# Optimization experiments

Hardware: AMD Instinct MI355X
Metric: run time of the kernel (lower is better)

## Reference

```python
import jax, jax.numpy as jnp
import numpy as np

N, S, E, H = 8, 1024, 1024, 16
DK = E // H

def setup_inputs() -> dict:
    key = jax.random.key(0)
    ks = jax.random.split(key, 10)
    s = 1.0 / np.sqrt(E)
    x = jax.random.normal(ks[0], (N, S, E), dtype=jnp.float32)
    attn_mask = jax.random.randint(ks[1], (N, S, S), 0, 2) == 1
    Wq = jax.random.normal(ks[2], (E, E), dtype=jnp.float32) * s
    Wk = jax.random.normal(ks[3], (E, E), dtype=jnp.float32) * s
    Wv = jax.random.normal(ks[4], (E, E), dtype=jnp.float32) * s
    Wo = jax.random.normal(ks[5], (E, E), dtype=jnp.float32) * s
    bq = jax.random.normal(ks[6], (E,), dtype=jnp.float32) * s
    bk = jax.random.normal(ks[7], (E,), dtype=jnp.float32) * s
    bv = jax.random.normal(ks[8], (E,), dtype=jnp.float32) * s
    bo = jax.random.normal(ks[9], (E,), dtype=jnp.float32) * s
    return {"x": x, "attn_mask": attn_mask, "Wq": Wq, "bq": bq, "Wk": Wk, "bk": bk,
            "Wv": Wv, "bv": bv, "Wo": Wo, "bo": bo}

def reference(x, attn_mask, Wq, bq, Wk, bk, Wv, bv, Wo, bo):
    n, s, e = x.shape
    # projections, split into heads: (N, H, S, DK)
    q = (x @ Wq + bq).reshape(n, s, H, DK).transpose(0, 2, 1, 3)
    k = (x @ Wk + bk).reshape(n, s, H, DK).transpose(0, 2, 1, 3)
    v = (x @ Wv + bv).reshape(n, s, H, DK).transpose(0, 2, 1, 3)
    logits = jnp.einsum("nhqd,nhkd->nhqk", q, k) / np.sqrt(DK).astype(np.float32)
    # mask==True positions are suppressed (masked_fill with -1e9)
    logits = jnp.where(attn_mask[:, None, :, :], jnp.float32(-1e9), logits)
    attn = jax.nn.softmax(logits, axis=-1)  # exp(log_softmax) == softmax
    o = jnp.einsum("nhqk,nhkd->nhqd", attn, v)
    o = o.transpose(0, 2, 1, 3).reshape(n, s, e)
    return o @ Wo + bo
```

## Files before the change

kernel.cpp:

```cpp
#include <hip/hip_runtime.h>
#include <hip/hip_bf16.h>

typedef unsigned short u16;
typedef unsigned int   u32;
typedef unsigned long long u64;

#define SEQ 1024
#define EMB 1024
#define NH  16
#define DKH 64

#define QSCALE 0.18033688f
#define SCLAMP 43.3f

typedef __attribute__((ext_vector_type(8))) short short8;
typedef __attribute__((ext_vector_type(4))) float floatx4;

__device__ __forceinline__ float b2f(u16 u) {
  return __uint_as_float(((u32)u) << 16);
}
__device__ __forceinline__ u16 f2b(float f) {
  u32 u = __float_as_uint(f);
  u32 r = u + 0x7fffu + ((u >> 16) & 1u);
  return (u16)(r >> 16);
}

__device__ __forceinline__ void glds16(const u16* g, u16* l) {
  __builtin_amdgcn_global_load_lds(
      (const __attribute__((address_space(1))) u32*)g,
      (__attribute__((address_space(3))) u32*)l, 16, 0, 0);
}

__global__ __launch_bounds__(256) void probe_inputs(const u32* __restrict__ A,
                                                    const u32* __restrict__ B,
                                                    int* __restrict__ flags) {
  __shared__ int mA, mB, mBig, xB16;
  if (threadIdx.x == 0) { mA = 0; mB = 0; mBig = 0; xB16 = 0; }
  __syncthreads();
  int la = 0, lb = 0;
  for (int i = threadIdx.x; i < 4096; i += 256) {
    if ((A[i] & 0xFEFEFEFEu) == 0) la++;
    if ((B[i] & 0xFEFEFEFEu) == 0) lb++;
  }
  atomicAdd(&mA, la); atomicAdd(&mB, lb);
  __syncthreads();
  const int xIsB = (mA > mB) ? 1 : 0;
  const u32* X = xIsB ? B : A;
  const u32* M = xIsB ? A : B;
  int big = 0, cnt = 0;
  for (int i = threadIdx.x; i < 4096; i += 256)
    if (M[i] > 1u) big = 1;
  for (int i = threadIdx.x; i < 2048; i += 256) {
    u16 v = (u16)(X[i] & 0xffffu);
    int e = (v >> 7) & 0xFF;
    if (e >= 110 && e <= 135) cnt++;
  }
  if (big) atomicOr(&mBig, 1);
  atomicAdd(&xB16, cnt);
  __syncthreads();
  if (threadIdx.x == 0) {
    flags[0] = xIsB;
    flags[1] = (xB16 > 1500) ? 1 : 0;
    flags[2] = mBig;
  }
}

__global__ __launch_bounds__(256) void convert_x(const void* __restrict__ bigA,
                                                 const void* __restrict__ bigB,
                                                 const int* __restrict__ flags,
                                                 u16* __restrict__ out) {
  const void* x = flags[0] ? bigB : bigA;
  int i = (blockIdx.x * 256 + threadIdx.x) * 4;
  if (flags[1]) {
    *(ushort4*)(out + i) = *(const ushort4*)((const u16*)x + i);
  } else {
    float4 v = *(const float4*)((const float*)x + i);
    ushort4 o;
    o.x = f2b(v.x); o.y = f2b(v.y); o.z = f2b(v.z); o.w = f2b(v.w);
    *(ushort4*)(out + i) = o;
  }
}

__global__ __launch_bounds__(256) void build_maskbits(const void* __restrict__ bigA,
                                                      const void* __restrict__ bigB,
                                                      const int* __restrict__ flags,
                                                      u32* __restrict__ out) {
  const void* mask = flags[0] ? bigA : bigB;
  const int mbyte = flags[2];
  const int t = threadIdx.x;
  const int lane = t & 63, w = t >> 6;
  const u64 base0 = (u64)blockIdx.x * 8192;
#pragma unroll 4
  for (int k = 0; k < 32; k++) {
    u64 idx = base0 + k * 256 + t;
    int v;
    if (mbyte) v = ((const unsigned char*)mask)[idx] == 0;
    else       v = ((const u32*)mask)[idx] == 0;
    u64 b = __ballot(v);
    if (lane == 0) {
      u64 wbase = (base0 + k * 256 + w * 64) >> 5;
      out[wbase]     = (u32)b;
      out[wbase + 1] = (u32)(b >> 32);
    }
  }
}

__global__ __launch_bounds__(256) void transpose_convert_w4(
    const void* __restrict__ w0, const void* __restrict__ w1,
    const void* __restrict__ w2, const void* __restrict__ w3,
    u16* __restrict__ outQKV, u16* __restrict__ outO,
    const int* __restrict__ flags) {
  __shared__ float tile[32][33];
  const int z = blockIdx.z;
  const void* in = (z == 0) ? w0 : (z == 1) ? w1 : (z == 2) ? w2 : w3;
  u16* out = (z < 3) ? (outQKV + (u64)z * EMB * EMB) : outO;
  const float scale = (z == 0) ? QSCALE : 1.0f;
  const int amode = flags[1];
  const int tx = threadIdx.x & 31;
  const int ty = threadIdx.x >> 5;
  const int bx = blockIdx.x * 32, by = blockIdx.y * 32;
  if (amode) {
    const u16* inb = (const u16*)in;
#pragma unroll
    for (int r = ty; r < 32; r += 8)
      tile[r][tx] = b2f(inb[(u64)(by + r) * EMB + bx + tx]);
  } else {
    const float* inf = (const float*)in;
#pragma unroll
    for (int r = ty; r < 32; r += 8)
      tile[r][tx] = inf[(u64)(by + r) * EMB + bx + tx];
  }
  __syncthreads();
#pragma unroll
  for (int r = ty; r < 32; r += 8)
    out[(u64)(bx + r) * EMB + by + tx] = f2b(tile[tx][r] * scale);
}

__global__ __launch_bounds__(256) void convert_biases(const void* b0, const void* b1,
                                                      const void* b2, const void* b3,
                                                      float* __restrict__ out,
                                                      const int* __restrict__ flags) {
  const void* ptrs[4] = {b0, b1, b2, b3};
  const void* p = ptrs[blockIdx.x];
  const float scale = (blockIdx.x == 0) ? QSCALE : 1.0f;
  const int amode = flags[1];
  for (int i = threadIdx.x; i < 1024; i += 256) {
    float v = amode ? b2f(((const u16*)p)[i]) : ((const float*)p)[i];
    out[blockIdx.x * 1024 + i] = v * scale;
  }
}

#define VTP 65
__global__ __launch_bounds__(256) void transpose_v(const u16* __restrict__ in,
                                                   u16* __restrict__ out) {
  __shared__ u16 tile[64 * VTP];
  const int t = threadIdx.x;
  const int s0 = blockIdx.x * 64;
  const u64 off = (u64)blockIdx.y * SEQ * DKH;
  const int row = t >> 2, c0 = (t & 3) * 16;
  const u16* ip = in + off + (u64)(s0 + row) * DKH + c0;
  *(uint4*)(&tile[row * VTP + c0])     = *(const uint4*)(ip);
  *(uint4*)(&tile[row * VTP + c0 + 8]) = *(const uint4*)(ip + 8);
  __syncthreads();
  const int d = t >> 2;
  u16 buf[16];
#pragma unroll
  for (int j = 0; j < 16; j++) buf[j] = tile[(c0 + j) * VTP + d];
  u16* op = out + off + (u64)d * SEQ + s0 + c0;
  *(uint4*)(op)     = *(uint4*)(&buf[0]);
  *(uint4*)(op + 8) = *(uint4*)(&buf[8]);
}


template <int OUTMODE>
__device__ __forceinline__ void gemm_core(
    const u16* __restrict__ X, const u16* __restrict__ Wt,
    const float* __restrict__ bias,
    u16* __restrict__ Qg, u16* __restrict__ Kg, u16* __restrict__ Vh,
    float* __restrict__ outf, int row0) {
  __shared__ __align__(16) u16 lds[2][(256 + 128) * 64];
  const int t = threadIdx.x;
  const int lane = t & 63;
  const int w = t >> 6;
  const int wr = w >> 1, wc = w & 1;
  const int l15 = lane & 15, l4 = lane >> 4;
  const int bM = blockIdx.x * 256, bN = blockIdx.y * 128;
  const int r7 = l15 & 7;
  const int cA = (l4 ^ r7) << 3;
  const int cB = (l4 ^ r7 ^ 4) << 3;

  floatx4 acc[4][4];
#pragma unroll
  for (int i = 0; i < 4; i++)
#pragma unroll
    for (int j = 0; j < 4; j++)
      acc[i][j] = (floatx4){0.f, 0.f, 0.f, 0.f};

  const int srow = w * 8 + (lane >> 3);
  const int schk = ((lane & 7) ^ (lane >> 3)) << 3;
  const u16* Ap = X + (u64)(row0 + bM + srow) * EMB + schk;
  const u16* Bp = Wt + (u64)(bN + srow) * EMB + schk;
  u16* Ad0 = &lds[0][w * 512];
  u16* Bd0 = &lds[0][16384 + w * 512];
  u16* Ad1 = &lds[1][w * 512];
  u16* Bd1 = &lds[1][16384 + w * 512];

  auto stage = [&](u16* Ad, u16* Bd, int k0) {
    glds16(Ap + k0, Ad);
    glds16(Ap + k0 + 64 * EMB, Ad + 4096);
    glds16(Ap + k0 + 128 * EMB, Ad + 8192);
    glds16(Ap + k0 + 192 * EMB, Ad + 12288);
    glds16(Bp + k0, Bd);
    glds16(Bp + k0 + 64 * EMB, Bd + 4096);
  };

  auto compute = [&](const u16* __restrict__ Ab, const u16* __restrict__ Bb) {
    short8 bf[4][2];
#pragma unroll
    for (int n = 0; n < 4; n++) {
      const int gr = (wc * 64 + n * 16 + l15) * 64;
      bf[n][0] = *(const short8*)(&Bb[gr + cA]);
      bf[n][1] = *(const short8*)(&Bb[gr + cB]);
    }
#pragma unroll
    for (int mh = 0; mh < 2; mh++) {
      short8 af[2][2];
#pragma unroll
      for (int m = 0; m < 2; m++) {
        const int fr = (wr * 64 + mh * 32 + m * 16 + l15) * 64;
        af[m][0] = *(const short8*)(&Ab[fr + cA]);
        af[m][1] = *(const short8*)(&Ab[fr + cB]);
      }
      __builtin_amdgcn_s_setprio(1);
#pragma unroll
      for (int m = 0; m < 2; m++)
#pragma unroll
        for (int n = 0; n < 4; n++) {
          acc[mh * 2 + m][n] = __builtin_amdgcn_mfma_f32_16x16x32_bf16(
              af[m][0], bf[n][0], acc[mh * 2 + m][n], 0, 0, 0);
          acc[mh * 2 + m][n] = __builtin_amdgcn_mfma_f32_16x16x32_bf16(
              af[m][1], bf[n][1], acc[mh * 2 + m][n], 0, 0, 0);
        }
      __builtin_amdgcn_s_setprio(0);
    }
  };

  stage(Ad0, Bd0, 0);
  for (int k0 = 0; k0 < EMB; k0 += 128) {
    stage(Ad1, Bd1, k0 + 64);
    asm volatile("s_waitcnt vmcnt(6)" ::: "memory");
    asm volatile("s_barrier" ::: "memory");
    compute(&lds[0][0], &lds[0][16384]);
    asm volatile("s_barrier" ::: "memory");
    if (k0 + 128 < EMB) {
      stage(Ad0, Bd0, k0 + 128);
      asm volatile("s_waitcnt vmcnt(6)" ::: "memory");
    } else {
      asm volatile("s_waitcnt vmcnt(0)" ::: "memory");
    }
    asm volatile("s_barrier" ::: "memory");
    compute(&lds[1][0], &lds[1][16384]);
    asm volatile("s_barrier" ::: "memory");
  }

  if (OUTMODE == 0) {
    const int sec = bN >> 10;
    u16* outp = (sec == 0) ? Qg : (sec == 1) ? Kg : Vh;
#pragma unroll
    for (int n = 0; n < 4; n++) {
      int col = bN + wc * 64 + n * 16 + l15;
      float bv = bias[col];
      int colh = col & 1023;
      int h = colh >> 6, d = colh & 63;
#pragma unroll
      for (int mt = 0; mt < 4; mt++) {
#pragma unroll
        for (int r = 0; r < 4; r++) {
          int row = bM + wr * 64 + mt * 16 + l4 * 4 + r;
          float v = acc[mt][n][r] + bv;
          int nb = row >> 10, s = row & 1023;
          outp[((u64)((nb * NH + h) * SEQ + s)) * DKH + d] = f2b(v);
        }
      }
    }
  } else {
#pragma unroll
    for (int n = 0; n < 4; n++) {
      int col = bN + wc * 64 + n * 16 + l15;
      float bv = bias[col];
#pragma unroll
      for (int mt = 0; mt < 4; mt++) {
#pragma unroll
        for (int r = 0; r < 4; r++) {
          int row = bM + wr * 64 + mt * 16 + l4 * 4 + r;
          outf[(u64)row * EMB + col] = acc[mt][n][r] + bv;
        }
      }
    }
  }
}

__global__ __launch_bounds__(512, 2) void gemm_qkv(
    const u16* __restrict__ X, const u16* __restrict__ Wt,
    const float* __restrict__ bias,
    u16* __restrict__ Qg, u16* __restrict__ Kg, u16* __restrict__ Vh,
    int row0) {
  gemm_core<0>(X, Wt, bias, Qg, Kg, Vh, nullptr, row0);
}

__global__ __launch_bounds__(512, 2) void gemm_out(
    const u16* __restrict__ X, const u16* __restrict__ Wt,
    const float* __restrict__ bias, float* __restrict__ out) {
  gemm_core<1>(X, Wt, bias, nullptr, nullptr, nullptr, out, 0);
}

__global__ __launch_bounds__(512, 8) void attn_mfma(
    const u16* __restrict__ Q, const u16* __restrict__ K,
    const u16* __restrict__ Vt, const u32* __restrict__ maskbits,
    int b0, u16* __restrict__ ctx) {
  __shared__ __align__(16) u16 Ks[2][64 * 64];
  __shared__ __align__(16) u16 Vs[64 * 64];
  __shared__ __align__(16) u16 Ps[128 * 64];

  const int t = threadIdx.x;
  const int lane = t & 63, w = t >> 6;
  const int l15 = lane & 15, l4 = lane >> 4;
  const int bid = blockIdx.x;
  const int h = bid & 15;
  const int qt = (bid >> 4) & 7;
  const int n = bid >> 7;
  const int nh = n * NH + h;
  const int q0 = qt * 128;
  const u64 hoff = (u64)nh * SEQ * DKH;

  const int r7 = l15 & 7;
  const int cA = (l4 ^ r7) << 3;
  const int cB = (l4 ^ r7 ^ 4) << 3;

  const int rt = w * 8 + (lane >> 3);
  const int chk = ((lane & 7) ^ (lane >> 3)) << 3;
  const u16* Kp = K + hoff + (u64)rt * DKH + chk;
  const u16* Vp = Vt + hoff + (u64)rt * SEQ + chk;
  const int ldsO = w * 512;

  short8 qf0, qf1;
  {
    const u16* qp = Q + hoff + (u64)(q0 + w * 16 + l15) * DKH + l4 * 8;
    qf0 = *(const short8*)(qp);
    qf1 = *(const short8*)(qp + 32);
  }

  short8 ones;
#pragma unroll
  for (int e = 0; e < 8; e++) ones[e] = (short)0x3F80;

  floatx4 o[4];
#pragma unroll
  for (int j = 0; j < 4; j++) o[j] = (floatx4){0.f, 0.f, 0.f, 0.f};
  floatx4 osum = (floatx4){0.f, 0.f, 0.f, 0.f};

  const u64 mrow = ((u64)((b0 + n) * SEQ + q0 + w * 16 + l15)) * 32;
  const int pq = w * 16 + l15;
  const int pc0 = (l4 * 4) ^ (r7 << 3);

  glds16(Kp, &Ks[0][ldsO]);
  glds16(Vp, &Vs[ldsO]);
  __syncthreads();

  int cur = 0;
  for (int kc = 0; kc < SEQ; kc += 64) {
    if (kc > 0) glds16(Vp + kc, &Vs[ldsO]);
    const int havek = (kc + 64 < SEQ);
    if (havek) glds16(Kp + (kc + 64) * DKH, &Ks[cur ^ 1][ldsO]);

    const u64 mbits = *(const u64*)(maskbits + mrow + (kc >> 5));
    const u16* Kc = &Ks[cur][0];

    __builtin_amdgcn_s_setprio(1);
#pragma unroll
    for (int j = 0; j < 4; j++) {
      floatx4 s = (floatx4){0.f, 0.f, 0.f, 0.f};
      const int rb = (j * 16 + l15) * 64;
      short8 kb0 = *(const short8*)(&Kc[rb + cA]);
      short8 kb1 = *(const short8*)(&Kc[rb + cB]);
      s = __builtin_amdgcn_mfma_f32_16x16x32_bf16(kb0, qf0, s, 0, 0, 0);
      s = __builtin_amdgcn_mfma_f32_16x16x32_bf16(kb1, qf1, s, 0, 0, 0);

      const u32 mj = (u32)(mbits >> (j * 16 + l4 * 4));
      float p0 = __uint_as_float(
          __float_as_uint(__builtin_amdgcn_exp2f(fminf(s[0], SCLAMP))) &
          (u32)__builtin_amdgcn_sbfe(mj, 0, 1));
      float p1 = __uint_as_float(
          __float_as_uint(__builtin_amdgcn_exp2f(fminf(s[1], SCLAMP))) &
          (u32)__builtin_amdgcn_sbfe(mj, 1, 1));
      float p2 = __uint_as_float(
          __float_as_uint(__builtin_amdgcn_exp2f(fminf(s[2], SCLAMP))) &
          (u32)__builtin_amdgcn_sbfe(mj, 2, 1));
      float p3 = __uint_as_float(
          __float_as_uint(__builtin_amdgcn_exp2f(fminf(s[3], SCLAMP))) &
          (u32)__builtin_amdgcn_sbfe(mj, 3, 1));

      uint2 pk;
      asm("v_cvt_pk_bf16_f32 %0, %1, %2" : "=v"(pk.x) : "v"(p0), "v"(p1));
      asm("v_cvt_pk_bf16_f32 %0, %1, %2" : "=v"(pk.y) : "v"(p2), "v"(p3));
      *(uint2*)(&Ps[pq * 64 + ((j * 16) ^ pc0)]) = pk;
    }

    if (havek) asm volatile("s_waitcnt vmcnt(1)" ::: "memory");
    else       asm volatile("s_waitcnt vmcnt(0)" ::: "memory");
    __builtin_amdgcn_s_barrier();

    short8 pa0 = *(const short8*)(&Ps[pq * 64 + cA]);
    short8 pa1 = *(const short8*)(&Ps[pq * 64 + cB]);
#pragma unroll
    for (int j = 0; j < 4; j++) {
      const int rb = (j * 16 + l15) * 64;
      short8 vb0 = *(const short8*)(&Vs[rb + cA]);
      short8 vb1 = *(const short8*)(&Vs[rb + cB]);
      o[j] = __builtin_amdgcn_mfma_f32_16x16x32_bf16(pa0, vb0, o[j], 0, 0, 0);
      o[j] = __builtin_amdgcn_mfma_f32_16x16x32_bf16(pa1, vb1, o[j], 0, 0, 0);
    }
    osum = __builtin_amdgcn_mfma_f32_16x16x32_bf16(pa0, ones, osum, 0, 0, 0);
    osum = __builtin_amdgcn_mfma_f32_16x16x32_bf16(pa1, ones, osum, 0, 0, 0);
    __builtin_amdgcn_s_setprio(0);

    __syncthreads();
    cur ^= 1;
  }

#pragma unroll
  for (int r = 0; r < 4; r++) {
    float invr = 1.0f / fmaxf(osum[r], 1e-30f);
    int q = q0 + w * 16 + l4 * 4 + r;
    u64 base = ((u64)(n * SEQ + q)) * EMB + h * DKH + l15;
#pragma unroll
    for (int j = 0; j < 4; j++)
      ctx[base + j * 16] = f2b(o[j][r] * invr);
  }
}

extern "C" void kernel_launch(void* const* d_in, const int* in_sizes, int n_in,
                              void* d_out, int out_size, void* d_ws, size_t ws_size,
                              hipStream_t stream) {
  int bigI[2] = {0, 1}, wI[4] = {2, 4, 6, 8}, bI[4] = {3, 5, 7, 9};
  int nb = 0, nw = 0, nbi = 0;
  for (int i = 0; i < n_in; i++) {
    if (in_sizes[i] == 8388608) { if (nb < 2) bigI[nb++] = i; }
    else if (in_sizes[i] == 1048576) { if (nw < 4) wI[nw++] = i; }
    else if (in_sizes[i] == 1024) { if (nbi < 4) bI[nbi++] = i; }
  }
  int oq = 0, ok = 1, ov = 2, oo = 3;
  if (nb == 2 && bigI[0] == 4 && bigI[1] == 9) { oq = 2; ok = 0; ov = 3; oo = 1; }

  const void* bigA = d_in[bigI[0]];
  const void* bigB = d_in[bigI[1]];
  const void* Wq = d_in[wI[oq]];
  const void* Wk = d_in[wI[ok]];
  const void* Wv = d_in[wI[ov]];
  const void* Wo = d_in[wI[oo]];
  const void* bq = d_in[bI[oq]];
  const void* bk = d_in[bI[ok]];
  const void* bv = d_in[bI[ov]];
  const void* bo = d_in[bI[oo]];

  char* ws = (char*)d_ws;
  u16* WtQKV = (u16*)ws;
  u16* WtO   = (u16*)(ws + (6ull << 20));
  float* biasf = (float*)(ws + (8ull << 20));
  int* flags = (int*)(ws + (8ull << 20) + 16384);
  u32* maskbits = (u32*)(ws + (8ull << 20) + 65536);
  u16* xb = (u16*)(ws + (10ull << 20));
  char* grp = ws + (26ull << 20);

  int G = 1;
  for (int g = 8; g >= 1; g >>= 1) {
    if (ws_size >= (26ull << 20) + (u64)g * (8ull << 20)) { G = g; break; }
  }
  const u64 gsz = (u64)G * (2ull << 20);
  u16* Qg = (u16*)grp;
  u16* Kg = (u16*)(grp + gsz);
  u16* Vh = (u16*)(grp + 2 * gsz);
  u16* Vt = (u16*)(grp + 3 * gsz);

  dim3 tb(256);

  probe_inputs<<<dim3(1), tb, 0, stream>>>((const u32*)bigA, (const u32*)bigB, flags);
  convert_x<<<dim3(8192), tb, 0, stream>>>(bigA, bigB, flags, xb);
  build_maskbits<<<dim3(1024), tb, 0, stream>>>(bigA, bigB, flags, maskbits);

  transpose_convert_w4<<<dim3(32, 32, 4), tb, 0, stream>>>(Wq, Wk, Wv, Wo, WtQKV, WtO, flags);
  convert_biases<<<dim3(4), tb, 0, stream>>>(bq, bk, bv, bo, biasf, flags);

  for (int b0 = 0; b0 < 8; b0 += G) {
    int row0 = b0 * 1024;
    gemm_qkv<<<dim3(4 * G, 24), dim3(512), 0, stream>>>(xb, WtQKV, biasf, Qg, Kg, Vh, row0);
    transpose_v<<<dim3(16, G * 16), tb, 0, stream>>>(Vh, Vt);

    attn_mfma<<<dim3(G * 16 * 8), dim3(512), 0, stream>>>(Qg, Kg, Vt, maskbits, b0, Vh);

    gemm_out<<<dim3(4 * G, 8), dim3(512), 0, stream>>>(Vh, WtO, biasf + 3072,
                                                       (float*)d_out + (u64)row0 * EMB);
  }
}
```

Before: 324.5 us.

## Double attention query tile to 256 rows per block to reuse K/V tiles

Each attention block now handles 256 query rows instead of 128, with each wave computing two 16-row query subtiles against the same K and V LDS tiles. This halves the number of blocks and the global/LDS traffic for K, V per query row, amortizing loads and barriers over more MFMA work. It doubles accumulator registers and P shared memory, and lowers launch-bound occupancy from 8 to 4 blocks per CU, with fewer blocks in flight.

```diff
diff --git a/kernel.cpp b/kernel.cpp
--- a/kernel.cpp
+++ b/kernel.cpp
@@ -314,23 +314,23 @@
   gemm_core<1>(X, Wt, bias, nullptr, nullptr, nullptr, out, 0);
 }
 
-__global__ __launch_bounds__(512, 8) void attn_mfma(
+__global__ __launch_bounds__(512, 4) void attn_mfma(
     const u16* __restrict__ Q, const u16* __restrict__ K,
     const u16* __restrict__ Vt, const u32* __restrict__ maskbits,
     int b0, u16* __restrict__ ctx) {
   __shared__ __align__(16) u16 Ks[2][64 * 64];
   __shared__ __align__(16) u16 Vs[64 * 64];
-  __shared__ __align__(16) u16 Ps[128 * 64];
+  __shared__ __align__(16) u16 Ps[256 * 64];
 
   const int t = threadIdx.x;
   const int lane = t & 63, w = t >> 6;
   const int l15 = lane & 15, l4 = lane >> 4;
   const int bid = blockIdx.x;
   const int h = bid & 15;
-  const int qt = (bid >> 4) & 7;
-  const int n = bid >> 7;
+  const int qt = (bid >> 4) & 3;
+  const int n = bid >> 6;
   const int nh = n * NH + h;
-  const int q0 = qt * 128;
+  const int q0 = qt * 256;
   const u64 hoff = (u64)nh * SEQ * DKH;
 
   const int r7 = l15 & 7;
@@ -343,24 +343,33 @@
   const u16* Vp = Vt + hoff + (u64)rt * SEQ + chk;
   const int ldsO = w * 512;
 
-  short8 qf0, qf1;
+  short8 qf[2][2];
   {
-    const u16* qp = Q + hoff + (u64)(q0 + w * 16 + l15) * DKH + l4 * 8;
-    qf0 = *(const short8*)(qp);
-    qf1 = *(const short8*)(qp + 32);
+    const u16* qpA = Q + hoff + (u64)(q0 + w * 32 + l15) * DKH + l4 * 8;
+    qf[0][0] = *(const short8*)(qpA);
+    qf[0][1] = *(const short8*)(qpA + 32);
+    const u16* qpB = qpA + 16 * DKH;
+    qf[1][0] = *(const short8*)(qpB);
+    qf[1][1] = *(const short8*)(qpB + 32);
   }
 
   short8 ones;
 #pragma unroll
   for (int e = 0; e < 8; e++) ones[e] = (short)0x3F80;
 
-  floatx4 o[4];
-#pragma unroll
-  for (int j = 0; j < 4; j++) o[j] = (floatx4){0.f, 0.f, 0.f, 0.f};
-  floatx4 osum = (floatx4){0.f, 0.f, 0.f, 0.f};
-
-  const u64 mrow = ((u64)((b0 + n) * SEQ + q0 + w * 16 + l15)) * 32;
-  const int pq = w * 16 + l15;
+  floatx4 o[2][4];
+#pragma unroll
+  for (int s = 0; s < 2; s++)
+#pragma unroll
+    for (int j = 0; j < 4; j++) o[s][j] = (floatx4){0.f, 0.f, 0.f, 0.f};
+  floatx4 osum[2];
+  osum[0] = (floatx4){0.f, 0.f, 0.f, 0.f};
+  osum[1] = (floatx4){0.f, 0.f, 0.f, 0.f};
+
+  const u64 mrow0 = ((u64)((b0 + n) * SEQ + q0 + w * 32 + l15)) * 32;
+  const u64 mrow1 = mrow0 + 16 * 32;
+  const int pq0 = w * 32 + l15;
+  const int pq1 = pq0 + 16;
   const int pc0 = (l4 * 4) ^ (r7 << 3);
 
   glds16(Kp, &Ks[0][ldsO]);
@@ -373,55 +382,83 @@
     const int havek = (kc + 64 < SEQ);
     if (havek) glds16(Kp + (kc + 64) * DKH, &Ks[cur ^ 1][ldsO]);
 
-    const u64 mbits = *(const u64*)(maskbits + mrow + (kc >> 5));
+    const u64 mb0 = *(const u64*)(maskbits + mrow0 + (kc >> 5));
+    const u64 mb1 = *(const u64*)(maskbits + mrow1 + (kc >> 5));
     const u16* Kc = &Ks[cur][0];
 
     __builtin_amdgcn_s_setprio(1);
 #pragma unroll
     for (int j = 0; j < 4; j++) {
-      floatx4 s = (floatx4){0.f, 0.f, 0.f, 0.f};
       const int rb = (j * 16 + l15) * 64;
       short8 kb0 = *(const short8*)(&Kc[rb + cA]);
       short8 kb1 = *(const short8*)(&Kc[rb + cB]);
-      s = __builtin_amdgcn_mfma_f32_16x16x32_bf16(kb0, qf0, s, 0, 0, 0);
-      s = __builtin_amdgcn_mfma_f32_16x16x32_bf16(kb1, qf1, s, 0, 0, 0);
-
-      const u32 mj = (u32)(mbits >> (j * 16 + l4 * 4));
-      float p0 = __uint_as_float(
-          __float_as_uint(__builtin_amdgcn_exp2f(fminf(s[0], SCLAMP))) &
-          (u32)__builtin_amdgcn_sbfe(mj, 0, 1));
-      float p1 = __uint_as_float(
-          __float_as_uint(__builtin_amdgcn_exp2f(fminf(s[1], SCLAMP))) &
-          (u32)__builtin_amdgcn_sbfe(mj, 1, 1));
-      float p2 = __uint_as_float(
-          __float_as_uint(__builtin_amdgcn_exp2f(fminf(s[2], SCLAMP))) &
-          (u32)__builtin_amdgcn_sbfe(mj, 2, 1));
-      float p3 = __uint_as_float(
-          __float_as_uint(__builtin_amdgcn_exp2f(fminf(s[3], SCLAMP))) &
-          (u32)__builtin_amdgcn_sbfe(mj, 3, 1));
-
-      uint2 pk;
-      asm("v_cvt_pk_bf16_f32 %0, %1, %2" : "=v"(pk.x) : "v"(p0), "v"(p1));
-      asm("v_cvt_pk_bf16_f32 %0, %1, %2" : "=v"(pk.y) : "v"(p2), "v"(p3));
-      *(uint2*)(&Ps[pq * 64 + ((j * 16) ^ pc0)]) = pk;
+      floatx4 s0 = (floatx4){0.f, 0.f, 0.f, 0.f};
+      floatx4 s1 = (floatx4){0.f, 0.f, 0.f, 0.f};
+      s0 = __builtin_amdgcn_mfma_f32_16x16x32_bf16(kb0, qf[0][0], s0, 0, 0, 0);
+      s0 = __builtin_amdgcn_mfma_f32_16x16x32_bf16(kb1, qf[0][1], s0, 0, 0, 0);
+      s1 = __builtin_amdgcn_mfma_f32_16x16x32_bf16(kb0, qf[1][0], s1, 0, 0, 0);
+      s1 = __builtin_amdgcn_mfma_f32_16x16x32_bf16(kb1, qf[1][1], s1, 0, 0, 0);
+
+      const u32 mj0 = (u32)(mb0 >> (j * 16 + l4 * 4));
+      const u32 mj1 = (u32)(mb1 >> (j * 16 + l4 * 4));
+      float p00 = __uint_as_float(
+          __float_as_uint(__builtin_amdgcn_exp2f(fminf(s0[0], SCLAMP))) &
+          (u32)__builtin_amdgcn_sbfe(mj0, 0, 1));
+      float p01 = __uint_as_float(
+          __float_as_uint(__builtin_amdgcn_exp2f(fminf(s0[1], SCLAMP))) &
+          (u32)__builtin_amdgcn_sbfe(mj0, 1, 1));
+      float p02 = __uint_as_float(
+          __float_as_uint(__builtin_amdgcn_exp2f(fminf(s0[2], SCLAMP))) &
+          (u32)__builtin_amdgcn_sbfe(mj0, 2, 1));
+      float p03 = __uint_as_float(
+          __float_as_uint(__builtin_amdgcn_exp2f(fminf(s0[3], SCLAMP))) &
+          (u32)__builtin_amdgcn_sbfe(mj0, 3, 1));
+      float p10 = __uint_as_float(
+          __float_as_uint(__builtin_amdgcn_exp2f(fminf(s1[0], SCLAMP))) &
+          (u32)__builtin_amdgcn_sbfe(mj1, 0, 1));
+      float p11 = __uint_as_float(
+          __float_as_uint(__builtin_amdgcn_exp2f(fminf(s1[1], SCLAMP))) &
+          (u32)__builtin_amdgcn_sbfe(mj1, 1, 1));
+      float p12 = __uint_as_float(
+          __float_as_uint(__builtin_amdgcn_exp2f(fminf(s1[2], SCLAMP))) &
+          (u32)__builtin_amdgcn_sbfe(mj1, 2, 1));
+      float p13 = __uint_as_float(
+          __float_as_uint(__builtin_amdgcn_exp2f(fminf(s1[3], SCLAMP))) &
+          (u32)__builtin_amdgcn_sbfe(mj1, 3, 1));
+
+      uint2 pk0, pk1;
+      asm("v_cvt_pk_bf16_f32 %0, %1, %2" : "=v"(pk0.x) : "v"(p00), "v"(p01));
+      asm("v_cvt_pk_bf16_f32 %0, %1, %2" : "=v"(pk0.y) : "v"(p02), "v"(p03));
+      asm("v_cvt_pk_bf16_f32 %0, %1, %2" : "=v"(pk1.x) : "v"(p10), "v"(p11));
+      asm("v_cvt_pk_bf16_f32 %0, %1, %2" : "=v"(pk1.y) : "v"(p12), "v"(p13));
+      const int pcol = (j * 16) ^ pc0;
+      *(uint2*)(&Ps[pq0 * 64 + pcol]) = pk0;
+      *(uint2*)(&Ps[pq1 * 64 + pcol]) = pk1;
     }
 
     if (havek) asm volatile("s_waitcnt vmcnt(1)" ::: "memory");
     else       asm volatile("s_waitcnt vmcnt(0)" ::: "memory");
     __builtin_amdgcn_s_barrier();
 
-    short8 pa0 = *(const short8*)(&Ps[pq * 64 + cA]);
-    short8 pa1 = *(const short8*)(&Ps[pq * 64 + cB]);
+    short8 pa[2][2];
+    pa[0][0] = *(const short8*)(&Ps[pq0 * 64 + cA]);
+    pa[0][1] = *(const short8*)(&Ps[pq0 * 64 + cB]);
+    pa[1][0] = *(const short8*)(&Ps[pq1 * 64 + cA]);
+    pa[1][1] = *(const short8*)(&Ps[pq1 * 64 + cB]);
 #pragma unroll
     for (int j = 0; j < 4; j++) {
       const int rb = (j * 16 + l15) * 64;
       short8 vb0 = *(const short8*)(&Vs[rb + cA]);
       short8 vb1 = *(const short8*)(&Vs[rb + cB]);
-      o[j] = __builtin_amdgcn_mfma_f32_16x16x32_bf16(pa0, vb0, o[j], 0, 0, 0);
-      o[j] = __builtin_amdgcn_mfma_f32_16x16x32_bf16(pa1, vb1, o[j], 0, 0, 0);
-    }
-    osum = __builtin_amdgcn_mfma_f32_16x16x32_bf16(pa0, ones, osum, 0, 0, 0);
-    osum = __builtin_amdgcn_mfma_f32_16x16x32_bf16(pa1, ones, osum, 0, 0, 0);
+      o[0][j] = __builtin_amdgcn_mfma_f32_16x16x32_bf16(pa[0][0], vb0, o[0][j], 0, 0, 0);
+      o[0][j] = __builtin_amdgcn_mfma_f32_16x16x32_bf16(pa[0][1], vb1, o[0][j], 0, 0, 0);
+      o[1][j] = __builtin_amdgcn_mfma_f32_16x16x32_bf16(pa[1][0], vb0, o[1][j], 0, 0, 0);
+      o[1][j] = __builtin_amdgcn_mfma_f32_16x16x32_bf16(pa[1][1], vb1, o[1][j], 0, 0, 0);
+    }
+    osum[0] = __builtin_amdgcn_mfma_f32_16x16x32_bf16(pa[0][0], ones, osum[0], 0, 0, 0);
+    osum[0] = __builtin_amdgcn_mfma_f32_16x16x32_bf16(pa[0][1], ones, osum[0], 0, 0, 0);
+    osum[1] = __builtin_amdgcn_mfma_f32_16x16x32_bf16(pa[1][0], ones, osum[1], 0, 0, 0);
+    osum[1] = __builtin_amdgcn_mfma_f32_16x16x32_bf16(pa[1][1], ones, osum[1], 0, 0, 0);
     __builtin_amdgcn_s_setprio(0);
 
     __syncthreads();
@@ -429,13 +466,16 @@
   }
 
 #pragma unroll
-  for (int r = 0; r < 4; r++) {
-    float invr = 1.0f / fmaxf(osum[r], 1e-30f);
-    int q = q0 + w * 16 + l4 * 4 + r;
-    u64 base = ((u64)(n * SEQ + q)) * EMB + h * DKH + l15;
-#pragma unroll
-    for (int j = 0; j < 4; j++)
-      ctx[base + j * 16] = f2b(o[j][r] * invr);
+  for (int s = 0; s < 2; s++) {
+#pragma unroll
+    for (int r = 0; r < 4; r++) {
+      float invr = 1.0f / fmaxf(osum[s][r], 1e-30f);
+      int q = q0 + w * 32 + s * 16 + l4 * 4 + r;
+      u64 base = ((u64)(n * SEQ + q)) * EMB + h * DKH + l15;
+#pragma unroll
+      for (int j = 0; j < 4; j++)
+        ctx[base + j * 16] = f2b(o[s][j][r] * invr);
+    }
   }
 }
 
@@ -496,7 +536,7 @@
     gemm_qkv<<<dim3(4 * G, 24), dim3(512), 0, stream>>>(xb, WtQKV, biasf, Qg, Kg, Vh, row0);
     transpose_v<<<dim3(16, G * 16), tb, 0, stream>>>(Vh, Vt);
 
-    attn_mfma<<<dim3(G * 16 * 8), dim3(512), 0, stream>>>(Qg, Kg, Vt, maskbits, b0, Vh);
+    attn_mfma<<<dim3(G * 16 * 4), dim3(512), 0, stream>>>(Qg, Kg, Vt, maskbits, b0, Vh);
 
     gemm_out<<<dim3(4 * G, 8), dim3(512), 0, stream>>>(Vh, WtO, biasf + 3072,
                                                        (float*)d_out + (u64)row0 * EMB);
```

After: 317.2 us. 2.3% less time.
